# Optimization experiments

Hardware: AMD Instinct MI355X
Metric: run time of the kernel (lower is better)

Reference implementation:

```python
import jax, jax.numpy as jnp
import numpy as np

# --- placement constants (mirror init_kwargs) ---
N = 500_000           # total nodes
M = 450_000           # movable nodes (first M)
NBX = 1024
NBY = 1024
XL = 0.0
YL = 0.0
BSX = 1.0
BSY = 1.0
K = 8                 # max bin span per axis for 'large' nodes (node size < 7*bin)


def setup_inputs() -> dict:
    key = jax.random.key(0)
    k1, k2, k3, k4, k5, k6 = jax.random.split(key, 6)
    # node centers strictly inside the die so large-node windows stay in range
    px = jax.random.uniform(k1, (N,), jnp.float32, 4.0, 1020.0)
    py = jax.random.uniform(k2, (N,), jnp.float32, 4.0, 1020.0)
    pos = jnp.concatenate([px, py])                      # [2N]
    potential_field = jax.random.normal(k3, (NBX, NBY), jnp.float32)
    rho_current = jax.random.uniform(k4, (NBX, NBY), jnp.float32, 0.1, 2.0)
    node_size_x = jax.random.uniform(k5, (N,), jnp.float32, 0.2, 6.0)
    node_size_y = jax.random.uniform(k6, (N,), jnp.float32, 0.2, 6.0)
    return {"pos": pos, "potential_field": potential_field,
            "rho_current": rho_current,
            "node_size_x": node_size_x, "node_size_y": node_size_y}


def _velocity_field(pot, hx, hy):
    # v = -grad(phi): 2nd-order central interior, 1st-order one-sided edges
    vx = -jnp.concatenate([(pot[1:2] - pot[0:1]) / hx,
                           (pot[2:] - pot[:-2]) / (2.0 * hx),
                           (pot[-1:] - pot[-2:-1]) / hx], axis=0)
    vy = -jnp.concatenate([(pot[:, 1:2] - pot[:, 0:1]) / hy,
                           (pot[:, 2:] - pot[:, :-2]) / (2.0 * hy),
                           (pot[:, -1:] - pot[:, -2:-1]) / hy], axis=1)
    return vx, vy


def _axis_window(center, size, lo, bs, nb):
    # per-node K-bin window of overlap lengths along one axis
    left = center - 0.5 * size
    right = center + 0.5 * size
    bmin = jnp.clip(jnp.floor((left - lo) / bs).astype(jnp.int32), 0, nb - 1)
    bmax = jnp.clip(jnp.floor((right - lo) / bs).astype(jnp.int32), 0, nb - 1)
    b = bmin[:, None] + jnp.arange(K, dtype=jnp.int32)        # [M,K]
    bin_left = lo + b.astype(jnp.float32) * bs
    ov = jnp.minimum(right[:, None], bin_left + bs) - jnp.maximum(left[:, None], bin_left)
    ov = jnp.where((b <= bmax[:, None]) & (ov > 0.0), ov, 0.0)
    return jnp.clip(b, 0, nb - 1), ov


def _interpolate_flux(pos, flux_x, flux_y, nsx, nsy):
    pos_x = pos[:N]
    pos_y = pos[N:]
    px = pos_x[:M]
    py = pos_y[:M]
    # --- bilinear path (small nodes) ---
    gx = (px - XL) / BSX
    gy = (py - YL) / BSY
    ix = jnp.clip(jnp.floor(gx).astype(jnp.int32), 0, NBX - 1)
    iy = jnp.clip(jnp.floor(gy).astype(jnp.int32), 0, NBY - 1)
    wx = jnp.clip(gx - ix.astype(jnp.float32), 0.0, 1.0)
    wy = jnp.clip(gy - iy.astype(jnp.float32), 0.0, 1.0)
    ix1 = jnp.clip(ix + 1, 0, NBX - 1)
    iy1 = jnp.clip(iy + 1, 0, NBY - 1)

    def bilerp(f):
        return ((1.0 - wx) * (1.0 - wy) * f[ix, iy] + wx * (1.0 - wy) * f[ix1, iy]
                + (1.0 - wx) * wy * f[ix, iy1] + wx * wy * f[ix1, iy1])

    bil_fx = bilerp(flux_x)
    bil_fy = bilerp(flux_y)
    # --- exact area-weighted path (large nodes), vectorized over K x K window ---
    w = nsx[:M]
    h = nsy[:M]
    bx, ox = _axis_window(px, w, XL, BSX, NBX)                # [M,K]
    by, oy = _axis_window(py, h, YL, BSY, NBY)                # [M,K]
    weights = ox[:, :, None] * oy[:, None, :]                 # [M,K,K] overlap areas
    fx_win = flux_x[bx[:, :, None], by[:, None, :]]           # [M,K,K]
    fy_win = flux_y[bx[:, :, None], by[:, None, :]]
    area = w * h
    safe_area = jnp.maximum(area, 1e-30)
    area_fx = jnp.where(area > 0.0, (fx_win * weights).sum((1, 2)) / safe_area, 0.0)
    area_fy = jnp.where(area > 0.0, (fy_win * weights).sum((1, 2)) / safe_area, 0.0)
    large = (w >= BSX) | (h >= BSY)
    gpx = jnp.where(large, area_fx, bil_fx)
    gpy = jnp.where(large, area_fy, bil_fy)
    grad_pos = jnp.zeros_like(pos)
    grad_pos = grad_pos.at[:M].set(gpx)
    grad_pos = grad_pos.at[N:N + M].set(gpy)
    return grad_pos


def reference(pos, potential_field, rho_current, node_size_x, node_size_y):
    vx, vy = _velocity_field(potential_field, BSX, BSY)
    bin_area = BSX * BSY
    energy = 0.5 * (rho_current * bin_area * (vx * vx + vy * vy)).sum().reshape(1)
    grad_pos = _interpolate_flux(pos, vx, vy, node_size_x, node_size_y)
    return energy, grad_pos
```

## Files before the change

kernel.cpp:

```cpp
#include <hip/hip_runtime.h>
#include <hip/hip_fp16.h>

#define NPART 500000
#define MPART 450000
#define NBXC 1024
#define NBYC 1024
#define KROW 7
#define NBLK_PART 1954

__global__ __launch_bounds__(256) void field_kernel(const float* __restrict__ pot,
                                                    const float* __restrict__ rho,
                                                    __half2* __restrict__ v,
                                                    float* __restrict__ partials) {
    const int idx = blockIdx.x * 256 + threadIdx.x;
    const int i  = idx >> 8;
    const int j4 = (idx & 255) << 2;

    const int ip = min(i + 1, NBXC - 1);
    const int im = max(i - 1, 0);
    const float sx = (ip - im == 2) ? 0.5f : 1.0f;

    const float4 c  = *reinterpret_cast<const float4*>(pot + i  * NBYC + j4);
    const float4 cu = *reinterpret_cast<const float4*>(pot + ip * NBYC + j4);
    const float4 cd = *reinterpret_cast<const float4*>(pot + im * NBYC + j4);
    const float  cl = pot[i * NBYC + max(j4 - 1, 0)];
    const float  cr = pot[i * NBYC + min(j4 + 4, NBYC - 1)];
    const float4 r4 = *reinterpret_cast<const float4*>(rho + i * NBYC + j4);

    const float vx0 = -(cu.x - cd.x) * sx;
    const float vx1 = -(cu.y - cd.y) * sx;
    const float vx2 = -(cu.z - cd.z) * sx;
    const float vx3 = -(cu.w - cd.w) * sx;

    const float vy0 = (j4 == 0)             ? -(c.y - c.x) : -(c.y - cl) * 0.5f;
    const float vy1 = -(c.z - c.x) * 0.5f;
    const float vy2 = -(c.w - c.y) * 0.5f;
    const float vy3 = (j4 + 3 == NBYC - 1)  ? -(c.w - c.z) : -(cr - c.z) * 0.5f;

    float4 st;
    st.x = __builtin_bit_cast(float, __floats2half2_rn(vx0, vy0));
    st.y = __builtin_bit_cast(float, __floats2half2_rn(vx1, vy1));
    st.z = __builtin_bit_cast(float, __floats2half2_rn(vx2, vy2));
    st.w = __builtin_bit_cast(float, __floats2half2_rn(vx3, vy3));
    *reinterpret_cast<float4*>(v + i * NBYC + j4) = st;

    float e = r4.x * (vx0 * vx0 + vy0 * vy0)
            + r4.y * (vx1 * vx1 + vy1 * vy1)
            + r4.z * (vx2 * vx2 + vy2 * vy2)
            + r4.w * (vx3 * vx3 + vy3 * vy3);
    #pragma unroll
    for (int off = 32; off > 0; off >>= 1) e += __shfl_down(e, off, 64);
    __shared__ float smem[4];
    const int lane = threadIdx.x & 63;
    const int wid  = threadIdx.x >> 6;
    if (lane == 0) smem[wid] = e;
    __syncthreads();
    if (threadIdx.x == 0) partials[blockIdx.x] = (smem[0] + smem[1]) + (smem[2] + smem[3]);
}

__global__ __launch_bounds__(256) void particle_kernel(const float* __restrict__ pos,
                                                       const float* __restrict__ nsx,
                                                       const float* __restrict__ nsy,
                                                       const __half2* __restrict__ v,
                                                       const float* __restrict__ partials,
                                                       float* __restrict__ out) {
    __shared__ float smem[4];

    if (blockIdx.x == NBLK_PART) {
        const int t = threadIdx.x;
        float e = (partials[t] + partials[t + 256]) + (partials[t + 512] + partials[t + 768]);
        #pragma unroll
        for (int off = 32; off > 0; off >>= 1) e += __shfl_down(e, off, 64);
        const int lane = t & 63;
        const int wid  = t >> 6;
        if (lane == 0) smem[wid] = e;
        __syncthreads();
        if (t == 0) out[0] = 0.5f * ((smem[0] + smem[1]) + (smem[2] + smem[3]));
        return;
    }

    const int i = blockIdx.x * 256 + threadIdx.x;
    if (i >= NPART) return;
    if (i >= MPART) {
        out[1 + i]         = 0.0f;
        out[1 + NPART + i] = 0.0f;
        return;
    }

    const float px = pos[i];
    const float py = pos[NPART + i];
    const float w  = nsx[i];
    const float h  = nsy[i];

    float gpx, gpy;
    const bool large = (w >= 1.0f) || (h >= 1.0f);
    if (!large) {
        int ix = min(max((int)floorf(px), 0), NBXC - 1);
        int iy = min(max((int)floorf(py), 0), NBYC - 1);
        const float wx = fminf(fmaxf(px - (float)ix, 0.0f), 1.0f);
        const float wy = fminf(fmaxf(py - (float)iy, 0.0f), 1.0f);
        const int ix1 = min(ix + 1, NBXC - 1);
        const int iy1 = min(iy + 1, NBYC - 1);
        const float2 f00 = __half22float2(v[ix  * NBYC + iy ]);
        const float2 f10 = __half22float2(v[ix1 * NBYC + iy ]);
        const float2 f01 = __half22float2(v[ix  * NBYC + iy1]);
        const float2 f11 = __half22float2(v[ix1 * NBYC + iy1]);
        const float w00 = (1.0f - wx) * (1.0f - wy);
        const float w10 = wx * (1.0f - wy);
        const float w01 = (1.0f - wx) * wy;
        const float w11 = wx * wy;
        gpx = w00 * f00.x + w10 * f10.x + w01 * f01.x + w11 * f11.x;
        gpy = w00 * f00.y + w10 * f10.y + w01 * f01.y + w11 * f11.y;
    } else {
        const float lx = px - 0.5f * w, rx = px + 0.5f * w;
        const float ly = py - 0.5f * h, ry = py + 0.5f * h;
        const int bminx = min(max((int)floorf(lx), 0), NBXC - 1);
        const int bmaxx = min(max((int)floorf(rx), 0), NBXC - 1);
        const int bminy = min(max((int)floorf(ly), 0), NBYC - 1);
        const int bmaxy = min(max((int)floorf(ry), 0), NBYC - 1);
        const int by0   = min(bminy & ~3, NBYC - 12);
        const int ncell = bmaxy - by0;

        float oy[12];
        #pragma unroll
        for (int k = 0; k < 12; ++k) {
            const int b = by0 + k;
            const float bl = (float)b;
            float ov = fminf(ry, bl + 1.0f) - fmaxf(ly, bl);
            oy[k] = (b <= bmaxy && ov > 0.0f) ? ov : 0.0f;
        }
        float ox[KROW];
        #pragma unroll
        for (int k = 0; k < KROW; ++k) {
            const int b = bminx + k;
            const float bl = (float)b;
            float ov = fminf(rx, bl + 1.0f) - fmaxf(lx, bl);
            ox[k] = (b <= bmaxx && ov > 0.0f) ? ov : 0.0f;
        }

        const float4 z = make_float4(0.0f, 0.0f, 0.0f, 0.0f);
        float afx = 0.0f, afy = 0.0f;

        auto rowptr = [&](int k) -> const float4* {
            const int bx = min(bminx + k, NBXC - 1);
            return reinterpret_cast<const float4*>(v + bx * NBYC + by0);
        };
        auto accum = [&](const float4& q0, const float4& q1, const float4& q2, float ov) {
            float sx = 0.0f, sy = 0.0f;
            const float* a0 = &q0.x;
            const float* a1 = &q1.x;
            const float* a2 = &q2.x;
            #pragma unroll
            for (int e = 0; e < 4; ++e) {
                const float2 f = __half22float2(__builtin_bit_cast(__half2, a0[e]));
                sx += f.x * oy[e];
                sy += f.y * oy[e];
            }
            #pragma unroll
            for (int e = 0; e < 4; ++e) {
                const float2 f = __half22float2(__builtin_bit_cast(__half2, a1[e]));
                sx += f.x * oy[4 + e];
                sy += f.y * oy[4 + e];
            }
            #pragma unroll
            for (int e = 0; e < 4; ++e) {
                const float2 f = __half22float2(__builtin_bit_cast(__half2, a2[e]));
                sx += f.x * oy[8 + e];
                sy += f.y * oy[8 + e];
            }
            afx += sx * ov;
            afy += sy * ov;
        };

        #pragma unroll
        for (int kp = 0; kp < 3; ++kp) {
            const int kA = 2 * kp, kB = 2 * kp + 1;
            const float ovA = ox[kA], ovB = ox[kB];
            float4 a0 = z, a1 = z, a2 = z, b0 = z, b1 = z, b2 = z;
            if (ovA > 0.0f) {
                const float4* rp = rowptr(kA);
                a0 = rp[0];
                if (ncell >= 4) a1 = rp[1];
                if (ncell >= 8) a2 = rp[2];
            }
            if (ovB > 0.0f) {
                const float4* rp = rowptr(kB);
                b0 = rp[0];
                if (ncell >= 4) b1 = rp[1];
                if (ncell >= 8) b2 = rp[2];
            }
            accum(a0, a1, a2, ovA);
            accum(b0, b1, b2, ovB);
        }
        {
            const float ov6 = ox[6];
            float4 a0 = z, a1 = z, a2 = z;
            if (ov6 > 0.0f) {
                const float4* rp = rowptr(6);
                a0 = rp[0];
                if (ncell >= 4) a1 = rp[1];
                if (ncell >= 8) a2 = rp[2];
            }
            accum(a0, a1, a2, ov6);
        }
        const float inv = 1.0f / fmaxf(w * h, 1e-30f);
        gpx = afx * inv;
        gpy = afy * inv;
    }
    out[1 + i]         = gpx;
    out[1 + NPART + i] = gpy;
}

extern "C" void kernel_launch(void* const* d_in, const int* in_sizes, int n_in,
                              void* d_out, int out_size, void* d_ws, size_t ws_size,
                              hipStream_t stream) {
    const float* pos = (const float*)d_in[0];
    const float* pot = (const float*)d_in[1];
    const float* rho = (const float*)d_in[2];
    const float* nsx = (const float*)d_in[3];
    const float* nsy = (const float*)d_in[4];
    float* out = (float*)d_out;

    __half2* v      = (__half2*)d_ws;
    float* partials = (float*)((char*)d_ws + (size_t)NBXC * NBYC * sizeof(__half2));

    field_kernel<<<(NBXC * NBYC / 4) / 256, 256, 0, stream>>>(pot, rho, v, partials);
    particle_kernel<<<NBLK_PART + 1, 256, 0, stream>>>(pos, nsx, nsy, v, partials, out);
}
```

Before: 31.81 us.

## Store velocity field in 4x4 tiled layout and simplify large-node gather loop

The half2 velocity field is now written in 4x4 bin tiles, so each 4x4 block of bins sits in 64 contiguous bytes. Both the bilinear path and the area-weighted path read from this tiled layout, which should improve cache-line locality for the 2D window gathers. The large-node loop is also restructured into a single unrolled loop that skips rows with zero overlap, replacing the paired-row prefetch scheme. This may reduce load-level parallelism, since rows are no longer loaded two at a time before accumulation.

Measured after the change: 38.42 us. +20.8%, slower.

```diff
diff --git a/kernel.cpp b/kernel.cpp
--- a/kernel.cpp
+++ b/kernel.cpp
@@ -8,13 +8,18 @@
 #define KROW 7
 #define NBLK_PART 1954
 
+__device__ __forceinline__ int tiled_idx(int x, int y) {
+    return (((x >> 2) * 256 + (y >> 2)) << 4) + ((x & 3) << 2) + (y & 3);
+}
+
 __global__ __launch_bounds__(256) void field_kernel(const float* __restrict__ pot,
                                                     const float* __restrict__ rho,
                                                     __half2* __restrict__ v,
                                                     float* __restrict__ partials) {
     const int idx = blockIdx.x * 256 + threadIdx.x;
     const int i  = idx >> 8;
-    const int j4 = (idx & 255) << 2;
+    const int ty = idx & 255;
+    const int j4 = ty << 2;
 
     const int ip = min(i + 1, NBXC - 1);
     const int im = max(i - 1, 0);
@@ -42,7 +47,7 @@
     st.y = __builtin_bit_cast(float, __floats2half2_rn(vx1, vy1));
     st.z = __builtin_bit_cast(float, __floats2half2_rn(vx2, vy2));
     st.w = __builtin_bit_cast(float, __floats2half2_rn(vx3, vy3));
-    *reinterpret_cast<float4*>(v + i * NBYC + j4) = st;
+    *reinterpret_cast<float4*>(v + ((((i >> 2) * 256 + ty) << 4) + ((i & 3) << 2))) = st;
 
     float e = r4.x * (vx0 * vx0 + vy0 * vy0)
             + r4.y * (vx1 * vx1 + vy1 * vy1)
@@ -101,10 +106,10 @@
         const float wy = fminf(fmaxf(py - (float)iy, 0.0f), 1.0f);
         const int ix1 = min(ix + 1, NBXC - 1);
         const int iy1 = min(iy + 1, NBYC - 1);
-        const float2 f00 = __half22float2(v[ix  * NBYC + iy ]);
-        const float2 f10 = __half22float2(v[ix1 * NBYC + iy ]);
-        const float2 f01 = __half22float2(v[ix  * NBYC + iy1]);
-        const float2 f11 = __half22float2(v[ix1 * NBYC + iy1]);
+        const float2 f00 = __half22float2(v[tiled_idx(ix,  iy )]);
+        const float2 f10 = __half22float2(v[tiled_idx(ix1, iy )]);
+        const float2 f01 = __half22float2(v[tiled_idx(ix,  iy1)]);
+        const float2 f11 = __half22float2(v[tiled_idx(ix1, iy1)]);
         const float w00 = (1.0f - wx) * (1.0f - wy);
         const float w10 = wx * (1.0f - wy);
         const float w01 = (1.0f - wx) * wy;
@@ -119,6 +124,7 @@
         const int bminy = min(max((int)floorf(ly), 0), NBYC - 1);
         const int bmaxy = min(max((int)floorf(ry), 0), NBYC - 1);
         const int by0   = min(bminy & ~3, NBYC - 12);
+        const int ty0   = by0 >> 2;
         const int ncell = bmaxy - by0;
 
         float oy[12];
@@ -129,27 +135,25 @@
             float ov = fminf(ry, bl + 1.0f) - fmaxf(ly, bl);
             oy[k] = (b <= bmaxy && ov > 0.0f) ? ov : 0.0f;
         }
-        float ox[KROW];
+
+        const float4 z = make_float4(0.0f, 0.0f, 0.0f, 0.0f);
+        float afx = 0.0f, afy = 0.0f;
         #pragma unroll
         for (int k = 0; k < KROW; ++k) {
             const int b = bminx + k;
             const float bl = (float)b;
             float ov = fminf(rx, bl + 1.0f) - fmaxf(lx, bl);
-            ox[k] = (b <= bmaxx && ov > 0.0f) ? ov : 0.0f;
-        }
-
-        const float4 z = make_float4(0.0f, 0.0f, 0.0f, 0.0f);
-        float afx = 0.0f, afy = 0.0f;
-
-        auto rowptr = [&](int k) -> const float4* {
-            const int bx = min(bminx + k, NBXC - 1);
-            return reinterpret_cast<const float4*>(v + bx * NBYC + by0);
-        };
-        auto accum = [&](const float4& q0, const float4& q1, const float4& q2, float ov) {
-            float sx = 0.0f, sy = 0.0f;
+            ov = (b <= bmaxx && ov > 0.0f) ? ov : 0.0f;
+            if (ov == 0.0f) continue;
+            const int bx = min(b, NBXC - 1);
+            const __half2* bp = v + ((((bx >> 2) * 256 + ty0) << 4) + ((bx & 3) << 2));
+            float4 q0 = *reinterpret_cast<const float4*>(bp);
+            float4 q1 = (ncell >= 4) ? *reinterpret_cast<const float4*>(bp + 16) : z;
+            float4 q2 = (ncell >= 8) ? *reinterpret_cast<const float4*>(bp + 32) : z;
             const float* a0 = &q0.x;
             const float* a1 = &q1.x;
             const float* a2 = &q2.x;
+            float sx = 0.0f, sy = 0.0f;
             #pragma unroll
             for (int e = 0; e < 4; ++e) {
                 const float2 f = __half22float2(__builtin_bit_cast(__half2, a0[e]));
@@ -170,38 +174,6 @@
             }
             afx += sx * ov;
             afy += sy * ov;
-        };
-
-        #pragma unroll
-        for (int kp = 0; kp < 3; ++kp) {
-            const int kA = 2 * kp, kB = 2 * kp + 1;
-            const float ovA = ox[kA], ovB = ox[kB];
-            float4 a0 = z, a1 = z, a2 = z, b0 = z, b1 = z, b2 = z;
-            if (ovA > 0.0f) {
-                const float4* rp = rowptr(kA);
-                a0 = rp[0];
-                if (ncell >= 4) a1 = rp[1];
-                if (ncell >= 8) a2 = rp[2];
-            }
-            if (ovB > 0.0f) {
-                const float4* rp = rowptr(kB);
-                b0 = rp[0];
-                if (ncell >= 4) b1 = rp[1];
-                if (ncell >= 8) b2 = rp[2];
-            }
-            accum(a0, a1, a2, ovA);
-            accum(b0, b1, b2, ovB);
-        }
-        {
-            const float ov6 = ox[6];
-            float4 a0 = z, a1 = z, a2 = z;
-            if (ov6 > 0.0f) {
-                const float4* rp = rowptr(6);
-                a0 = rp[0];
-                if (ncell >= 4) a1 = rp[1];
-                if (ncell >= 8) a2 = rp[2];
-            }
-            accum(a0, a1, a2, ov6);
         }
         const float inv = 1.0f / fmaxf(w * h, 1e-30f);
         gpx = afx * inv;
```
